# Optimization experiments

Measured on AMD Instinct MI355X. Metric: run time of the kernel, lower is better.

## Reference

```python
import jax, jax.numpy as jnp
import numpy as np

B, S, D, H = 64, 197, 768, 12
HD = D // H  # 64
WIN = 14
NUM_REL = (2 * WIN - 1) ** 2 + 3  # 732


def _build_rel_index():
    ch = np.arange(WIN)
    coords = np.stack(np.meshgrid(ch, ch, indexing='ij'))  # [2, W, W]
    flat = coords.reshape(2, -1)  # [2, W*W]
    rel = flat[:, :, None] - flat[:, None, :]  # [2, W*W, W*W]
    rel = rel.transpose(1, 2, 0).astype(np.int64)
    rel[:, :, 0] += WIN - 1
    rel[:, :, 1] += WIN - 1
    rel[:, :, 0] *= 2 * WIN - 1
    idx = np.zeros((WIN * WIN + 1, WIN * WIN + 1), dtype=np.int64)
    idx[1:, 1:] = rel.sum(-1)
    idx[0, :] = NUM_REL - 3
    idx[:, 0] = NUM_REL - 2
    idx[0, 0] = NUM_REL - 1
    return idx


def setup_inputs() -> dict:
    key = jax.random.key(0)
    ks = jax.random.split(key, 7)
    s = 0.02
    return {
        'hidden_states': jax.random.normal(ks[0], (B, S, D), jnp.float32),
        'wq': jax.random.normal(ks[1], (D, D), jnp.float32) * s,
        'bq': jax.random.normal(ks[2], (D,), jnp.float32) * s,
        'wk': jax.random.normal(ks[3], (D, D), jnp.float32) * s,  # key has no bias in BEiT
        'wv': jax.random.normal(ks[4], (D, D), jnp.float32) * s,
        'bv': jax.random.normal(ks[5], (D,), jnp.float32) * s,
        'bias_table': jax.random.normal(ks[6], (NUM_REL, H), jnp.float32) * s,
        'rel_index': jnp.asarray(_build_rel_index(), jnp.int32),
    }


def reference(hidden_states, wq, bq, wk, wv, bv, bias_table, rel_index):
    def heads(x):  # [B,S,D] -> [B,H,S,HD]
        return x.reshape(B, S, H, HD).transpose(0, 2, 1, 3)

    q = heads(hidden_states @ wq.T + bq)
    k = heads(hidden_states @ wk.T)
    v = heads(hidden_states @ wv.T + bv)

    scale = 1.0 / jnp.sqrt(jnp.asarray(HD, hidden_states.dtype))
    scores = jnp.einsum('bhqd,bhkd->bhqk', q, k) * scale  # [B,H,S,S]

    # relative position bias: [S,S,H] -> [1,H,S,S]
    rel_bias = bias_table[rel_index].transpose(2, 0, 1)[None]
    scores = scores + rel_bias

    probs = jax.nn.softmax(scores, axis=-1)
    ctx = jnp.einsum('bhqk,bhkd->bhqd', probs, v)  # [B,H,S,HD]
    return ctx.transpose(0, 2, 1, 3).reshape(B, S, D)
```

## Files before the change

### kernel.cpp

```cpp
#include <hip/hip_runtime.h>


#define S_LEN 197
#define HEADS 12
#define HDIM 64
#define DMODEL 768
#define BATCH 64
#define MROWS (BATCH * S_LEN)
#define MPAD 12672
#define NCOLS (3 * DMODEL)
#define KDIM DMODEL
#define NQT 13
#define NTILE (NCOLS / 128)
#define MTILE (MPAD / 128)

typedef __attribute__((ext_vector_type(8))) short short8;
typedef __attribute__((ext_vector_type(4))) float floatx4;

#define GLD16(gp, lp)                                                                  \
  __builtin_amdgcn_global_load_lds(                                                    \
      (const __attribute__((address_space(1))) unsigned int*)(gp),                     \
      (__attribute__((address_space(3))) unsigned int*)(lp), 16, 0, 0)

__device__ __forceinline__ ushort f2bf(float f) {
  union { float f; unsigned int i; } x;
  x.f = f;
  unsigned int r = x.i + 0x7fffu + ((x.i >> 16) & 1u);
  return (ushort)(r >> 16);
}

__global__ __launch_bounds__(256) void k_prep(
    const float* __restrict__ hs, const float* __restrict__ wq,
    const float* __restrict__ wk, const float* __restrict__ wv,
    const float* __restrict__ bt, const int* __restrict__ ridx,
    ushort* __restrict__ hbf, ushort* __restrict__ wbf, float* __restrict__ biasF) {
  int gid = blockIdx.x * 256 + threadIdx.x;
  int gsz = gridDim.x * 256;
  for (int i = gid; i < MPAD * KDIM / 8; i += gsz) {
    int base = i * 8;
    int row = base / KDIM;
    ushort o[8];
    if (row < MROWS) {
      const float* s = hs + (size_t)base;
#pragma unroll
      for (int e = 0; e < 8; ++e) o[e] = f2bf(s[e]);
    } else {
#pragma unroll
      for (int e = 0; e < 8; ++e) o[e] = 0;
    }
    *(uint4*)&hbf[base] = *(const uint4*)o;
  }
  for (int i = gid; i < NCOLS * KDIM / 8; i += gsz) {
    int base = i * 8;
    int row = base / KDIM;
    int col = base - row * KDIM;
    const float* src = (row < DMODEL) ? &wq[(size_t)row * KDIM]
                       : (row < 2 * DMODEL) ? &wk[(size_t)(row - DMODEL) * KDIM]
                                            : &wv[(size_t)(row - 2 * DMODEL) * KDIM];
    ushort o[8];
#pragma unroll
    for (int e = 0; e < 8; ++e) o[e] = f2bf(src[col + e]);
    *(uint4*)&wbf[base] = *(const uint4*)o;
  }
  for (int idx = gid; idx < HEADS * NQT * NQT * 64; idx += gsz) {
    int lane = idx & 63;
    int rest = idx >> 6;
    int t = rest % NQT;
    int rest2 = rest / NQT;
    int qt = rest2 % NQT;
    int h = rest2 / NQT;
    int l16 = lane & 15, quad = lane >> 4;
    int q = qt * 16 + l16;
    floatx4 v;
#pragma unroll
    for (int r = 0; r < 4; ++r) {
      int key = t * 16 + quad * 4 + r;
      float x = -1e30f;
      if (q < S_LEN && key < S_LEN) x = bt[ridx[q * S_LEN + key] * HEADS + h];
      v[r] = x;
    }
    *(floatx4*)&biasF[(size_t)idx * 4] = v;
  }
}

__global__ __launch_bounds__(256) void k_gemm_qkv(
    const ushort* __restrict__ A, const ushort* __restrict__ W,
    const float* __restrict__ bq, const float* __restrict__ bv,
    ushort* __restrict__ Cb) {
  __shared__ __align__(16) ushort SH[128 * 128];
  ushort* As = SH;
  ushort* Bs = SH + 128 * 32;
  int tid = threadIdx.x;
  int wave = tid >> 6, lane = tid & 63;
  int quad = lane >> 4, l16 = lane & 15;

  int linear = blockIdx.y * NTILE + blockIdx.x;
  int m_t, n_t;
  if (linear < 1776) {
    int g = (linear & 7) * 222 + (linear >> 3);
    m_t = g / NTILE;
    n_t = g - m_t * NTILE;
  } else {
    m_t = linear / NTILE;
    n_t = linear - m_t * NTILE;
  }
  int m0 = m_t * 128, n0 = n_t * 128;
  int wm = (wave & 1) * 64, wn = (wave >> 1) * 64;
  int swz = (quad ^ ((l16 >> 1) & 3)) << 3;

  floatx4 acc[4][4];
  floatx4 z = {0.f, 0.f, 0.f, 0.f};
#pragma unroll
  for (int i = 0; i < 4; ++i)
#pragma unroll
    for (int j = 0; j < 4; ++j) acc[i][j] = z;

  int p0 = wave * 128 + lane;
  for (int kb = 0; kb < KDIM; kb += 32) {
    const ushort* Arow = A + (size_t)m0 * KDIM + kb;
    const ushort* Brow = W + (size_t)n0 * KDIM + kb;
#pragma unroll
    for (int s = 0; s < 2; ++s) {
      int p = p0 + s * 64;
      int r = p >> 2;
      int kc = ((p & 3) ^ ((p >> 3) & 3)) << 3;
      GLD16(&Arow[(size_t)r * KDIM + kc], &As[p * 8]);
      GLD16(&Brow[(size_t)r * KDIM + kc], &Bs[p * 8]);
    }
    __syncthreads();
    short8 af[4], bfr[4];
#pragma unroll
    for (int i = 0; i < 4; ++i) {
      af[i] = *(const short8*)(&As[(wm + i * 16 + l16) * 32 + swz]);
      bfr[i] = *(const short8*)(&Bs[(wn + i * 16 + l16) * 32 + swz]);
    }
#pragma unroll
    for (int i = 0; i < 4; ++i)
#pragma unroll
      for (int j = 0; j < 4; ++j)
        acc[i][j] = __builtin_amdgcn_mfma_f32_16x16x32_bf16(af[i], bfr[j], acc[i][j], 0, 0, 0);
    __syncthreads();
  }

#pragma unroll
  for (int j = 0; j < 4; ++j) {
    int coln = wn + j * 16 + l16;
    int col = n0 + coln;
    float bias = (col < DMODEL) ? bq[col] : ((col >= 2 * DMODEL) ? bv[col - 2 * DMODEL] : 0.f);
    float scl = (col < DMODEL) ? 0.125f : 1.0f;
#pragma unroll
    for (int i = 0; i < 4; ++i)
#pragma unroll
      for (int r = 0; r < 4; ++r) {
        int row = wm + i * 16 + quad * 4 + r;
        int ch = (coln >> 3) ^ (row & 7);
        SH[row * 128 + (ch << 3) + (coln & 7)] = f2bf((acc[i][j][r] + bias) * scl);
      }
  }
  __syncthreads();
#pragma unroll
  for (int p = 0; p < 2; ++p) {
    int row = p * 64 + wave * 16 + (lane >> 2);
    int q4 = lane & 3;
    ushort* gC = Cb + (size_t)(m0 + row) * NCOLS + n0;
#pragma unroll
    for (int c = 0; c < 4; ++c) {
      int cp = c * 4 + q4;
      int ch = cp ^ (row & 7);
      *(uint4*)&gC[cp * 8] = *(const uint4*)&SH[row * 128 + (ch << 3)];
    }
  }
}

__global__ __launch_bounds__(256) void k_attn_mfma(
    const ushort* __restrict__ Cb0, const float* __restrict__ biasF,
    float* __restrict__ out) {
  __shared__ __align__(16) ushort Vt[HDIM * 256];
  __shared__ __align__(16) ushort Ka[NQT * 2 * 512];
  int bh = blockIdx.x;
  int b = bh / HEADS, h = bh - b * HEADS;
  int tid = threadIdx.x;
  int wave = tid >> 6, lane = tid & 63;
  int quad = lane >> 4, l16 = lane & 15;
  const ushort* Cb = Cb0 + (size_t)b * S_LEN * NCOLS;
  const int qoff = h * HDIM, koff = DMODEL + h * HDIM, voff = 2 * DMODEL + h * HDIM;

  {
    uint4 z4 = {0u, 0u, 0u, 0u};
    for (int i = tid; i < HDIM * 256 / 8; i += 256) ((uint4*)Vt)[i] = z4;
  }
  __syncthreads();
  for (int idx = tid; idx < S_LEN * 32; idx += 256) {
    int key = idx >> 5, dp = (idx & 31) * 2;
    unsigned int v = *(const unsigned int*)&Cb[(size_t)key * NCOLS + voff + dp];
    int ch = key >> 3, co = key & 7;
    Vt[dp * 256 + ((ch ^ (dp & 7)) << 3) + co] = (ushort)(v & 0xffffu);
    Vt[(dp + 1) * 256 + ((ch ^ ((dp + 1) & 7)) << 3) + co] = (ushort)(v >> 16);
  }
  for (int th = wave; th < NQT * 2; th += 4) {
    int t = th >> 1, half = th & 1;
    short8 kf = *(const short8*)&Cb[(size_t)(t * 16 + l16) * NCOLS + koff + half * 32 + quad * 8];
    *(short8*)&Ka[th * 512 + lane * 8] = kf;
  }
  __syncthreads();

  for (int qt = wave; qt < NQT; qt += 4) {
    int q0 = qt * 16;
    int q = q0 + l16;
    short8 qb0 = *(const short8*)&Cb[(size_t)q * NCOLS + qoff + quad * 8];
    short8 qb1 = *(const short8*)&Cb[(size_t)q * NCOLS + qoff + 32 + quad * 8];
    const float* bF = biasF + ((size_t)((h * NQT + qt) * NQT) * 64 + lane) * 4;

    floatx4 sacc[NQT];
#pragma unroll
    for (int t = 0; t < NQT; ++t) {
      floatx4 cin = *(const floatx4*)&bF[t * 256];
      short8 ka0 = *(const short8*)&Ka[(t * 2 + 0) * 512 + lane * 8];
      short8 ka1 = *(const short8*)&Ka[(t * 2 + 1) * 512 + lane * 8];
      floatx4 s1 = __builtin_amdgcn_mfma_f32_16x16x32_bf16(ka0, qb0, cin, 0, 0, 0);
      sacc[t] = __builtin_amdgcn_mfma_f32_16x16x32_bf16(ka1, qb1, s1, 0, 0, 0);
    }

    float mx = -3e38f;
#pragma unroll
    for (int t = 0; t < NQT; ++t)
#pragma unroll
      for (int r = 0; r < 4; ++r) mx = fmaxf(mx, sacc[t][r]);
    mx = fmaxf(mx, __shfl_xor(mx, 16));
    mx = fmaxf(mx, __shfl_xor(mx, 32));
    float sum = 0.f;
    unsigned int pbf[NQT][2];
#pragma unroll
    for (int t = 0; t < NQT; ++t) {
      float e0 = __expf(sacc[t][0] - mx), e1 = __expf(sacc[t][1] - mx);
      float e2 = __expf(sacc[t][2] - mx), e3 = __expf(sacc[t][3] - mx);
      sum += (e0 + e1) + (e2 + e3);
      union { float f; unsigned int u; } a, bb, c, d;
      a.f = e0; bb.f = e1; c.f = e2; d.f = e3;
      pbf[t][0] = ((a.u + 0x8000u) >> 16) | ((bb.u + 0x8000u) & 0xffff0000u);
      pbf[t][1] = ((c.u + 0x8000u) >> 16) | ((d.u + 0x8000u) & 0xffff0000u);
    }
    sum += __shfl_xor(sum, 16);
    sum += __shfl_xor(sum, 32);
    float inv = 1.f / sum;

    floatx4 oacc[4];
    floatx4 zz = {0.f, 0.f, 0.f, 0.f};
#pragma unroll
    for (int dt = 0; dt < 4; ++dt) oacc[dt] = zz;
    int sel0 = ((quad & 1) * 2) * 16 + l16;
    int sel1 = sel0 + 16;
#pragma unroll
    for (int kk = 0; kk < 7; ++kk) {
      unsigned int u0 = 0, u1 = 0, u2 = 0, u3 = 0;
#pragma unroll
      for (int half = 0; half < 2; ++half) {
        int t = 2 * kk + half;
        if (t < NQT) {
          unsigned int v0 = __shfl((int)pbf[t][0], sel0);
          unsigned int v1 = __shfl((int)pbf[t][1], sel0);
          unsigned int v2 = __shfl((int)pbf[t][0], sel1);
          unsigned int v3 = __shfl((int)pbf[t][1], sel1);
          if ((quad >> 1) == half) { u0 = v0; u1 = v1; u2 = v2; u3 = v3; }
        }
      }
      union { uint4 u; short8 s; } pf;
      pf.u.x = u0; pf.u.y = u1; pf.u.z = u2; pf.u.w = u3;
#pragma unroll
      for (int dt = 0; dt < 4; ++dt) {
        int d = dt * 16 + l16;
        short8 vf = *(const short8*)&Vt[d * 256 + (((kk * 4 + quad) ^ (d & 7)) << 3)];
        oacc[dt] = __builtin_amdgcn_mfma_f32_16x16x32_bf16(vf, pf.s, oacc[dt], 0, 0, 0);
      }
    }

    if (q < S_LEN) {
      float* og = out + ((size_t)b * S_LEN + q) * DMODEL + h * HDIM + quad * 4;
#pragma unroll
      for (int dt = 0; dt < 4; ++dt) {
        floatx4 o = oacc[dt];
        float4 st = make_float4(o[0] * inv, o[1] * inv, o[2] * inv, o[3] * inv);
        *(float4*)&og[dt * 16] = st;
      }
    }
  }
}

extern "C" void kernel_launch(void* const* d_in, const int* in_sizes, int n_in,
                              void* d_out, int out_size, void* d_ws, size_t ws_size,
                              hipStream_t stream) {
  const float* hs = (const float*)d_in[0];
  const float* wq = (const float*)d_in[1];
  const float* bq = (const float*)d_in[2];
  const float* wk = (const float*)d_in[3];
  const float* wv = (const float*)d_in[4];
  const float* bv = (const float*)d_in[5];
  const float* bt = (const float*)d_in[6];
  const int* ridx = (const int*)d_in[7];
  float* out = (float*)d_out;

  ushort* hbf = (ushort*)d_ws;
  ushort* wbf = hbf + (size_t)MPAD * KDIM;
  ushort* Cb = wbf + (size_t)NCOLS * KDIM;
  float* biasF = (float*)(Cb + (size_t)MPAD * NCOLS);

  k_prep<<<2048, 256, 0, stream>>>(hs, wq, wk, wv, bt, ridx, hbf, wbf, biasF);
  k_gemm_qkv<<<dim3(NTILE, MTILE), 256, 0, stream>>>(hbf, wbf, bq, bv, Cb);
  k_attn_mfma<<<BATCH * HEADS, 256, 0, stream>>>(Cb, biasF, out);
}
```

Before: 237.6 us.

## Deepen QKV GEMM K-tile to 64 and stage attention output through LDS

```diff
diff --git a/kernel.cpp b/kernel.cpp
--- a/kernel.cpp
+++ b/kernel.cpp
@@ -9,10 +9,11 @@
 #define MROWS (BATCH * S_LEN)
 #define MPAD 12672
 #define NCOLS (3 * DMODEL)
-#define KDIM DMODEL
+#define KDIM 768
 #define NQT 13
 #define NTILE (NCOLS / 128)
 #define MTILE (MPAD / 128)
+#define OS_ST 76
 
 typedef __attribute__((ext_vector_type(8))) short short8;
 typedef __attribute__((ext_vector_type(4))) float floatx4;
@@ -89,7 +90,7 @@
     ushort* __restrict__ Cb) {
   __shared__ __align__(16) ushort SH[128 * 128];
   ushort* As = SH;
-  ushort* Bs = SH + 128 * 32;
+  ushort* Bs = SH + 128 * 64;
   int tid = threadIdx.x;
   int wave = tid >> 6, lane = tid & 63;
   int quad = lane >> 4, l16 = lane & 15;
@@ -106,7 +107,6 @@
   }
   int m0 = m_t * 128, n0 = n_t * 128;
   int wm = (wave & 1) * 64, wn = (wave >> 1) * 64;
-  int swz = (quad ^ ((l16 >> 1) & 3)) << 3;
 
   floatx4 acc[4][4];
   floatx4 z = {0.f, 0.f, 0.f, 0.f};
@@ -115,30 +115,33 @@
 #pragma unroll
     for (int j = 0; j < 4; ++j) acc[i][j] = z;
 
-  int p0 = wave * 128 + lane;
-  for (int kb = 0; kb < KDIM; kb += 32) {
+  for (int kb = 0; kb < KDIM; kb += 64) {
     const ushort* Arow = A + (size_t)m0 * KDIM + kb;
     const ushort* Brow = W + (size_t)n0 * KDIM + kb;
 #pragma unroll
-    for (int s = 0; s < 2; ++s) {
-      int p = p0 + s * 64;
-      int r = p >> 2;
-      int kc = ((p & 3) ^ ((p >> 3) & 3)) << 3;
+    for (int s = 0; s < 4; ++s) {
+      int p = s * 256 + tid;
+      int r = p >> 3;
+      int kc = (((p & 7) ^ (r & 7))) << 3;
       GLD16(&Arow[(size_t)r * KDIM + kc], &As[p * 8]);
       GLD16(&Brow[(size_t)r * KDIM + kc], &Bs[p * 8]);
     }
     __syncthreads();
-    short8 af[4], bfr[4];
-#pragma unroll
-    for (int i = 0; i < 4; ++i) {
-      af[i] = *(const short8*)(&As[(wm + i * 16 + l16) * 32 + swz]);
-      bfr[i] = *(const short8*)(&Bs[(wn + i * 16 + l16) * 32 + swz]);
-    }
-#pragma unroll
-    for (int i = 0; i < 4; ++i)
-#pragma unroll
-      for (int j = 0; j < 4; ++j)
-        acc[i][j] = __builtin_amdgcn_mfma_f32_16x16x32_bf16(af[i], bfr[j], acc[i][j], 0, 0, 0);
+#pragma unroll
+    for (int kk = 0; kk < 2; ++kk) {
+      int coff = ((kk * 4 + quad) ^ (l16 & 7)) << 3;
+      short8 af[4], bfr[4];
+#pragma unroll
+      for (int i = 0; i < 4; ++i) {
+        af[i] = *(const short8*)(&As[(wm + i * 16 + l16) * 64 + coff]);
+        bfr[i] = *(const short8*)(&Bs[(wn + i * 16 + l16) * 64 + coff]);
+      }
+#pragma unroll
+      for (int i = 0; i < 4; ++i)
+#pragma unroll
+        for (int j = 0; j < 4; ++j)
+          acc[i][j] = __builtin_amdgcn_mfma_f32_16x16x32_bf16(af[i], bfr[j], acc[i][j], 0, 0, 0);
+    }
     __syncthreads();
   }
 
@@ -177,6 +180,7 @@
     float* __restrict__ out) {
   __shared__ __align__(16) ushort Vt[HDIM * 256];
   __shared__ __align__(16) ushort Ka[NQT * 2 * 512];
+  __shared__ __align__(16) float Os[4 * 16 * OS_ST];
   int bh = blockIdx.x;
   int b = bh / HEADS, h = bh - b * HEADS;
   int tid = threadIdx.x;
@@ -204,6 +208,7 @@
   }
   __syncthreads();
 
+  float* Osw = Os + wave * 16 * OS_ST;
   for (int qt = wave; qt < NQT; qt += 4) {
     int q0 = qt * 16;
     int q = q0 + l16;
@@ -274,14 +279,20 @@
       }
     }
 
-    if (q < S_LEN) {
-      float* og = out + ((size_t)b * S_LEN + q) * DMODEL + h * HDIM + quad * 4;
-#pragma unroll
-      for (int dt = 0; dt < 4; ++dt) {
-        floatx4 o = oacc[dt];
-        float4 st = make_float4(o[0] * inv, o[1] * inv, o[2] * inv, o[3] * inv);
-        *(float4*)&og[dt * 16] = st;
-      }
+#pragma unroll
+    for (int dt = 0; dt < 4; ++dt) {
+      floatx4 o;
+#pragma unroll
+      for (int r = 0; r < 4; ++r) o[r] = oacc[dt][r] * inv;
+      *(floatx4*)&Osw[l16 * OS_ST + dt * 16 + quad * 4] = o;
+    }
+    float* outg = out + ((size_t)b * S_LEN) * DMODEL + h * HDIM;
+#pragma unroll
+    for (int i = 0; i < 4; ++i) {
+      int ql = i * 4 + (lane >> 4);
+      float4 o4 = *(const float4*)&Osw[ql * OS_ST + (lane & 15) * 4];
+      int qg = q0 + ql;
+      if (qg < S_LEN) *(float4*)&outg[(size_t)qg * DMODEL + (lane & 15) * 4] = o4;
     }
   }
 }
```

After: 238.1 us. No clear change (+0.2%).
